# Kernel optimization log

Measured on AMD Instinct MI355X. Metric: run time of the kernel, lower is better.

## Reference

```python
import jax, jax.numpy as jnp
import numpy as np

QMAX = 127.0  # int8 symmetric range used by quanto absmax quantizer


def setup_inputs() -> dict:
    key = jax.random.key(0)
    k1, k2, k3 = jax.random.split(key, 3)
    x = jax.random.normal(k1, (4, 2048, 1600), dtype=jnp.float32)
    weight = jax.random.normal(k2, (1600, 6400), dtype=jnp.float32) * 0.02  # Conv1D init std=0.02
    bias = jax.random.normal(k3, (6400,), dtype=jnp.float32) * 0.02
    in_scale = jnp.float32(0.02)   # calibration scale for activations
    out_scale = jnp.float32(0.05)  # calibration scale for outputs
    return {"x": x, "weight": weight, "bias": bias, "in_scale": in_scale, "out_scale": out_scale}


def reference(x, weight, bias, in_scale, out_scale):
    # --- quantize input to int8 with the fixed in_scale (QTensor.quantize) ---
    x_q = jnp.clip(jnp.round(x / in_scale), -128, 127).astype(jnp.int32)
    # --- quantize weight to int8 with absmax scale (QTensor.quantize default) ---
    w_scale = jnp.max(jnp.abs(weight)) / QMAX
    w_q = jnp.clip(jnp.round(weight / w_scale), -128, 127).astype(jnp.int32)
    # --- quantize bias to int32 at the accumulator scale ---
    bias_scale = in_scale * w_scale
    b_q = jnp.round(bias / bias_scale).astype(jnp.int32)
    # --- int32-accumulated addmm: [B*S, nx] @ [nx, nf] + [nf] ---
    bsz = x.shape[:-1]
    nx = x.shape[-1]
    acc_i32 = jnp.matmul(x_q.reshape(-1, nx), w_q,
                         preferred_element_type=jnp.int32) + b_q[None, :]
    # --- rescale int32 accumulator (scale=bias_scale) to int8 at out_scale ---
    out_q = jnp.clip(jnp.round(acc_i32.astype(jnp.float32) * (bias_scale / out_scale)),
                     -128, 127).astype(jnp.int8)
    # return the dequantized value the downstream layer would see
    out = out_q.astype(jnp.float32) * out_scale
    return out.reshape(*bsz, -1)
```

## Files before the change

### kernel.cpp

```cpp
#include <hip/hip_runtime.h>


#define M_DIM 8192
#define K_DIM 1600
#define N_DIM 6400
#define QMAXF 127.0f

typedef __attribute__((ext_vector_type(4))) int int4v;


__device__ __forceinline__ void load_lds16(const void* gptr, void* lptr) {
    __builtin_amdgcn_global_load_lds((__attribute__((address_space(1))) void*)gptr,
                                     (__attribute__((address_space(3))) void*)lptr,
                                     16, 0, 0);
}

__global__ void wmax_kernel(const float* __restrict__ w,
                            unsigned int* __restrict__ wmax_bits, int n4) {
    __shared__ float smax[4];
    const float4* w4 = (const float4*)w;
    int i = blockIdx.x * blockDim.x + threadIdx.x;
    int stride = gridDim.x * blockDim.x;
    float m = 0.0f;
    for (; i < n4; i += stride) {
        float4 v = w4[i];
        m = fmaxf(m, fmaxf(fmaxf(fabsf(v.x), fabsf(v.y)),
                           fmaxf(fabsf(v.z), fabsf(v.w))));
    }
#pragma unroll
    for (int off = 32; off > 0; off >>= 1)
        m = fmaxf(m, __shfl_down(m, off, 64));
    const int wave = threadIdx.x >> 6;
    if ((threadIdx.x & 63) == 0) smax[wave] = m;
    __syncthreads();
    if (threadIdx.x == 0) {
        float mm = fmaxf(fmaxf(smax[0], smax[1]), fmaxf(smax[2], smax[3]));
        atomicMax(wmax_bits, __float_as_uint(mm));
    }
}

__global__ void quantx_kernel(const float* __restrict__ x, signed char* __restrict__ xq,
                              const float* __restrict__ in_scale_p, int n4) {
    int i = blockIdx.x * blockDim.x + threadIdx.x;
    if (i >= n4) return;
    float s = *in_scale_p;
    float4 v = ((const float4*)x)[i];
    float a = fminf(fmaxf(rintf(v.x / s), -128.0f), 127.0f);
    float b = fminf(fmaxf(rintf(v.y / s), -128.0f), 127.0f);
    float c = fminf(fmaxf(rintf(v.z / s), -128.0f), 127.0f);
    float d = fminf(fmaxf(rintf(v.w / s), -128.0f), 127.0f);
    char4 packed = make_char4((signed char)a, (signed char)b,
                              (signed char)c, (signed char)d);
    ((char4*)xq)[i] = packed;
}

__global__ void quantw_kernel(const float* __restrict__ w, signed char* __restrict__ wT,
                              const unsigned int* __restrict__ wmax_bits) {
    __shared__ signed char tile[64 * 80];
    const float wscale = __uint_as_float(*wmax_bits) / QMAXF;
    const int n0 = blockIdx.x * 64;
    const int k0 = blockIdx.y * 64;
    const int tid = threadIdx.x;
    const int nn = tid & 63;
    const int kb = tid >> 6;
#pragma unroll
    for (int p = 0; p < 16; ++p) {
        const int kk = p * 4 + kb;
        float v = w[(size_t)(k0 + kk) * N_DIM + n0 + nn];
        float q = fminf(fmaxf(rintf(v / wscale), -128.0f), 127.0f);
        tile[nn * 80 + kk] = (signed char)q;
    }
    __syncthreads();
    const int n_loc = tid >> 2;
    const int kq = tid & 3;
    int4v val = *(const int4v*)&tile[n_loc * 80 + kq * 16];
    *(int4v*)&wT[(size_t)(n0 + n_loc) * K_DIM + k0 + kq * 16] = val;
}

__global__ __launch_bounds__(256, 3) void gemm_i8_kernel(
        const signed char* __restrict__ xq, const signed char* __restrict__ wTq,
        const float* __restrict__ bias, const unsigned int* __restrict__ wmax_bits,
        const float* __restrict__ in_scale_p, const float* __restrict__ out_scale_p,
        float* __restrict__ out) {
    __shared__ signed char A_lds[3][128 * 64];
    __shared__ signed char B_lds[3][128 * 64];

    const int tid   = threadIdx.x;
    const int wave  = tid >> 6;
    const int lane  = tid & 63;
    const int quad  = lane >> 4;
    const int l15   = lane & 15;
    const int waveM = wave >> 1;
    const int waveN = wave & 1;

    const int gid   = blockIdx.x;
    const int xcd   = gid & 7;
    const int idx   = gid >> 3;
    const int n_blk = idx >> 3;
    const int m_blk = (xcd << 3) | (idx & 7);

    const int blockN0 = n_blk * 128;
    const int blockM0 = m_blk * 128;

    const signed char* Ag = xq  + (size_t)blockM0 * K_DIM;
    const signed char* Bg = wTq + (size_t)blockN0 * K_DIM;

    const int srow = wave * 16 + (lane >> 2);
    const int scol = (((lane & 3) ^ ((lane >> 3) & 3)) * 16);

    int4v acc[4][4];
    const int4v zero4 = {0, 0, 0, 0};
#pragma unroll
    for (int i = 0; i < 4; ++i)
#pragma unroll
        for (int j = 0; j < 4; ++j) acc[i][j] = zero4;

    const int rchunk = (quad ^ ((l15 >> 1) & 3)) * 16;

    const int NT = K_DIM / 64;

    auto STAGE = [&](int sb, int kt) {
        const int kof = kt * 64;
#pragma unroll
        for (int t = 0; t < 2; ++t) {
            const int r = t * 64 + srow;
            load_lds16(Ag + (size_t)r * K_DIM + kof + scol,
                       &A_lds[sb][(t * 64 + wave * 16) * 64]);
            load_lds16(Bg + (size_t)r * K_DIM + kof + scol,
                       &B_lds[sb][(t * 64 + wave * 16) * 64]);
        }
    };

    auto COMPUTE = [&](int cb) {
        int4v a[4], b[4];
#pragma unroll
        for (int mt = 0; mt < 4; ++mt)
            a[mt] = *(const int4v*)&A_lds[cb][(waveM * 64 + mt * 16 + l15) * 64 + rchunk];
#pragma unroll
        for (int nt = 0; nt < 4; ++nt)
            b[nt] = *(const int4v*)&B_lds[cb][(waveN * 64 + nt * 16 + l15) * 64 + rchunk];
#pragma unroll
        for (int mt = 0; mt < 4; ++mt)
#pragma unroll
            for (int nt = 0; nt < 4; ++nt)
                acc[mt][nt] = __builtin_amdgcn_mfma_i32_16x16x64_i8(a[mt], b[nt],
                                                                    acc[mt][nt], 0, 0, 0);
    };

    STAGE(0, 0);
    STAGE(1, 1);

    int cb = 0;
    for (int t = 0; t < NT - 2; ++t) {
        const int sb = (cb == 0) ? 2 : cb - 1;
        STAGE(sb, t + 2);
        asm volatile("s_waitcnt vmcnt(8)" ::: "memory");
        __builtin_amdgcn_s_barrier();
        __builtin_amdgcn_sched_barrier(0);
        COMPUTE(cb);
        asm volatile("s_waitcnt lgkmcnt(0)" ::: "memory");
        __builtin_amdgcn_sched_barrier(0);
        __builtin_amdgcn_s_barrier();
        cb = (cb == 2) ? 0 : cb + 1;
    }

    asm volatile("s_waitcnt vmcnt(4)" ::: "memory");
    __builtin_amdgcn_s_barrier();
    __builtin_amdgcn_sched_barrier(0);
    COMPUTE(cb);
    cb = (cb == 2) ? 0 : cb + 1;

    asm volatile("s_waitcnt vmcnt(0)" ::: "memory");
    __builtin_amdgcn_s_barrier();
    __builtin_amdgcn_sched_barrier(0);
    COMPUTE(cb);

    const float s_in  = *in_scale_p;
    const float s_out = *out_scale_p;
    const float wscale = __uint_as_float(*wmax_bits) / QMAXF;
    const float bias_scale = s_in * wscale;
    const float ratio = bias_scale / s_out;

#pragma unroll
    for (int nt = 0; nt < 4; ++nt) {
        const int col = blockN0 + waveN * 64 + nt * 16 + l15;
        const int bq = (int)rintf(bias[col] / bias_scale);
#pragma unroll
        for (int mt = 0; mt < 4; ++mt) {
#pragma unroll
            for (int r = 0; r < 4; ++r) {
                const int row = blockM0 + waveM * 64 + mt * 16 + quad * 4 + r;
                const int av = acc[mt][nt][r] + bq;
                float f = rintf((float)av * ratio);
                f = fminf(fmaxf(f, -128.0f), 127.0f);
                __builtin_nontemporal_store(f * s_out, &out[(size_t)row * N_DIM + col]);
            }
        }
    }
}

extern "C" void kernel_launch(void* const* d_in, const int* in_sizes, int n_in,
                              void* d_out, int out_size, void* d_ws, size_t ws_size,
                              hipStream_t stream) {
    const float* x         = (const float*)d_in[0];
    const float* w         = (const float*)d_in[1];
    const float* bias      = (const float*)d_in[2];
    const float* in_scale  = (const float*)d_in[3];
    const float* out_scale = (const float*)d_in[4];
    float* out = (float*)d_out;

    unsigned char* ws = (unsigned char*)d_ws;
    unsigned int* wmax_bits = (unsigned int*)ws;
    signed char* xq  = (signed char*)(ws + 256);
    signed char* wTq = (signed char*)(ws + 256 + (size_t)M_DIM * K_DIM);

    hipMemsetAsync(d_ws, 0, 256, stream);

    wmax_kernel<<<320, 256, 0, stream>>>(w, wmax_bits, (K_DIM * N_DIM) / 4);

    quantx_kernel<<<(M_DIM * K_DIM / 4 + 255) / 256, 256, 0, stream>>>(
        x, xq, in_scale, M_DIM * K_DIM / 4);

    dim3 wgrid(N_DIM / 64, K_DIM / 64);
    quantw_kernel<<<wgrid, 256, 0, stream>>>(w, wTq, wmax_bits);

    gemm_i8_kernel<<<3200, 256, 0, stream>>>(xq, wTq, bias, wmax_bits,
                                             in_scale, out_scale, out);
}
```

Baseline: 396.5 us.

## Switch GEMM to 32x32x32 int8 MFMA and fold memset into quantx kernel

The GEMM inner loop now uses 32x32x32 int8 MFMA tiles (2x2 per wave) instead of 16x16x64 (4x4 per wave), with matching LDS fragment addressing and swizzle plus a reworked epilogue row mapping. The aim is fewer MFMA issues and fewer LDS reads per k-step. The quantize-x kernel now handles 16 elements per thread in a grid-stride loop with 16-byte stores. It also zeroes the wmax word, which removes the separate memset call. The risks are the more complex fragment/epilogue index mapping and wider, less coalesced epilogue stores.

```diff
diff --git a/kernel.cpp b/kernel.cpp
--- a/kernel.cpp
+++ b/kernel.cpp
@@ -7,12 +7,35 @@
 #define QMAXF 127.0f
 
 typedef __attribute__((ext_vector_type(4))) int int4v;
+typedef __attribute__((ext_vector_type(16))) int int16v;
 
 
 __device__ __forceinline__ void load_lds16(const void* gptr, void* lptr) {
     __builtin_amdgcn_global_load_lds((__attribute__((address_space(1))) void*)gptr,
                                      (__attribute__((address_space(3))) void*)lptr,
                                      16, 0, 0);
+}
+
+__global__ void quantx_kernel(const float* __restrict__ x, signed char* __restrict__ xq,
+                              const float* __restrict__ in_scale_p,
+                              unsigned int* __restrict__ wmax_bits, int n16) {
+    if (blockIdx.x == 0 && threadIdx.x == 0) *wmax_bits = 0u;
+    const float s = *in_scale_p;
+    const float4* x4 = (const float4*)x;
+    int i = blockIdx.x * blockDim.x + threadIdx.x;
+    const int stride = gridDim.x * blockDim.x;
+    for (; i < n16; i += stride) {
+        signed char tmp[16];
+#pragma unroll
+        for (int j = 0; j < 4; ++j) {
+            float4 v = x4[(size_t)i * 4 + j];
+            tmp[j * 4 + 0] = (signed char)fminf(fmaxf(rintf(v.x / s), -128.0f), 127.0f);
+            tmp[j * 4 + 1] = (signed char)fminf(fmaxf(rintf(v.y / s), -128.0f), 127.0f);
+            tmp[j * 4 + 2] = (signed char)fminf(fmaxf(rintf(v.z / s), -128.0f), 127.0f);
+            tmp[j * 4 + 3] = (signed char)fminf(fmaxf(rintf(v.w / s), -128.0f), 127.0f);
+        }
+        *(int4v*)&xq[(size_t)i * 16] = *(const int4v*)tmp;
+    }
 }
 
 __global__ void wmax_kernel(const float* __restrict__ w,
@@ -39,21 +62,6 @@
     }
 }
 
-__global__ void quantx_kernel(const float* __restrict__ x, signed char* __restrict__ xq,
-                              const float* __restrict__ in_scale_p, int n4) {
-    int i = blockIdx.x * blockDim.x + threadIdx.x;
-    if (i >= n4) return;
-    float s = *in_scale_p;
-    float4 v = ((const float4*)x)[i];
-    float a = fminf(fmaxf(rintf(v.x / s), -128.0f), 127.0f);
-    float b = fminf(fmaxf(rintf(v.y / s), -128.0f), 127.0f);
-    float c = fminf(fmaxf(rintf(v.z / s), -128.0f), 127.0f);
-    float d = fminf(fmaxf(rintf(v.w / s), -128.0f), 127.0f);
-    char4 packed = make_char4((signed char)a, (signed char)b,
-                              (signed char)c, (signed char)d);
-    ((char4*)xq)[i] = packed;
-}
-
 __global__ void quantw_kernel(const float* __restrict__ w, signed char* __restrict__ wT,
                               const unsigned int* __restrict__ wmax_bits) {
     __shared__ signed char tile[64 * 80];
@@ -88,8 +96,8 @@
     const int tid   = threadIdx.x;
     const int wave  = tid >> 6;
     const int lane  = tid & 63;
-    const int quad  = lane >> 4;
-    const int l15   = lane & 15;
+    const int l31   = lane & 31;
+    const int hi    = lane >> 5;
     const int waveM = wave >> 1;
     const int waveN = wave & 1;
 
@@ -108,14 +116,15 @@
     const int srow = wave * 16 + (lane >> 2);
     const int scol = (((lane & 3) ^ ((lane >> 3) & 3)) * 16);
 
-    int4v acc[4][4];
-    const int4v zero4 = {0, 0, 0, 0};
-#pragma unroll
-    for (int i = 0; i < 4; ++i)
-#pragma unroll
-        for (int j = 0; j < 4; ++j) acc[i][j] = zero4;
-
-    const int rchunk = (quad ^ ((l15 >> 1) & 3)) * 16;
+    int16v acc[2][2];
+#pragma unroll
+    for (int mi = 0; mi < 2; ++mi)
+#pragma unroll
+        for (int ni = 0; ni < 2; ++ni)
+#pragma unroll
+            for (int r = 0; r < 16; ++r) acc[mi][ni][r] = 0;
+
+    const int rswz = (l31 >> 1) & 3;
 
     const int NT = K_DIM / 64;
 
@@ -132,19 +141,25 @@
     };
 
     auto COMPUTE = [&](int cb) {
-        int4v a[4], b[4];
-#pragma unroll
-        for (int mt = 0; mt < 4; ++mt)
-            a[mt] = *(const int4v*)&A_lds[cb][(waveM * 64 + mt * 16 + l15) * 64 + rchunk];
-#pragma unroll
-        for (int nt = 0; nt < 4; ++nt)
-            b[nt] = *(const int4v*)&B_lds[cb][(waveN * 64 + nt * 16 + l15) * 64 + rchunk];
-#pragma unroll
-        for (int mt = 0; mt < 4; ++mt)
-#pragma unroll
-            for (int nt = 0; nt < 4; ++nt)
-                acc[mt][nt] = __builtin_amdgcn_mfma_i32_16x16x64_i8(a[mt], b[nt],
-                                                                    acc[mt][nt], 0, 0, 0);
+        int4v a[2][2], b[2][2];
+#pragma unroll
+        for (int ks = 0; ks < 2; ++ks)
+#pragma unroll
+            for (int ti = 0; ti < 2; ++ti) {
+                const int ch = ((((ks << 1) | hi) ^ rswz) << 4);
+                a[ks][ti] = *(const int4v*)
+                    &A_lds[cb][(waveM * 64 + ti * 32 + l31) * 64 + ch];
+                b[ks][ti] = *(const int4v*)
+                    &B_lds[cb][(waveN * 64 + ti * 32 + l31) * 64 + ch];
+            }
+#pragma unroll
+        for (int ks = 0; ks < 2; ++ks)
+#pragma unroll
+            for (int mi = 0; mi < 2; ++mi)
+#pragma unroll
+                for (int ni = 0; ni < 2; ++ni)
+                    acc[mi][ni] = __builtin_amdgcn_mfma_i32_32x32x32_i8(
+                        a[ks][mi], b[ks][ni], acc[mi][ni], 0, 0, 0);
     };
 
     STAGE(0, 0);
@@ -182,15 +197,16 @@
     const float ratio = bias_scale / s_out;
 
 #pragma unroll
-    for (int nt = 0; nt < 4; ++nt) {
-        const int col = blockN0 + waveN * 64 + nt * 16 + l15;
+    for (int ni = 0; ni < 2; ++ni) {
+        const int col = blockN0 + waveN * 64 + ni * 32 + l31;
         const int bq = (int)rintf(bias[col] / bias_scale);
 #pragma unroll
-        for (int mt = 0; mt < 4; ++mt) {
-#pragma unroll
-            for (int r = 0; r < 4; ++r) {
-                const int row = blockM0 + waveM * 64 + mt * 16 + quad * 4 + r;
-                const int av = acc[mt][nt][r] + bq;
+        for (int mi = 0; mi < 2; ++mi) {
+#pragma unroll
+            for (int reg = 0; reg < 16; ++reg) {
+                const int row = blockM0 + waveM * 64 + mi * 32 +
+                                (reg & 3) + 8 * (reg >> 2) + 4 * hi;
+                const int av = acc[mi][ni][reg] + bq;
                 float f = rintf((float)av * ratio);
                 f = fminf(fmaxf(f, -128.0f), 127.0f);
                 __builtin_nontemporal_store(f * s_out, &out[(size_t)row * N_DIM + col]);
@@ -214,12 +230,10 @@
     signed char* xq  = (signed char*)(ws + 256);
     signed char* wTq = (signed char*)(ws + 256 + (size_t)M_DIM * K_DIM);
 
-    hipMemsetAsync(d_ws, 0, 256, stream);
+    quantx_kernel<<<2048, 256, 0, stream>>>(x, xq, in_scale, wmax_bits,
+                                            M_DIM * K_DIM / 16);
 
     wmax_kernel<<<320, 256, 0, stream>>>(w, wmax_bits, (K_DIM * N_DIM) / 4);
-
-    quantx_kernel<<<(M_DIM * K_DIM / 4 + 255) / 256, 256, 0, stream>>>(
-        x, xq, in_scale, M_DIM * K_DIM / 4);
 
     dim3 wgrid(N_DIM / 64, K_DIM / 64);
     quantw_kernel<<<wgrid, 256, 0, stream>>>(w, wTq, wmax_bits);
```

Result: faster. 386.8 us (-2.5%).
